# Performance work log

Measured on AMD Instinct MI355X. Metric: run time of the kernel, lower is better.

## Reference

```python
import jax, jax.numpy as jnp
import numpy as np

N_EMBED = 1024
CUTOFFS = [20000, 40000, 200000]
N_VOCAB = 267735
N_EMBEDS = [1024, 256, 64, 16]  # n_embed // 4**i
N_TOKENS = 1024
STARTS = [0] + CUTOFFS
ENDS = CUTOFFS + [N_VOCAB]


def setup_inputs() -> dict:
    key = jax.random.key(0)
    ks = jax.random.split(key, 16)
    s = 0.02
    inp = {}
    inp["hidden"] = jax.random.normal(ks[0], (N_TOKENS, N_EMBED), jnp.float32)
    inp["target"] = jax.random.randint(ks[1], (N_TOKENS,), 0, N_VOCAB)
    # head: layers[0] = Linear(1024, 20000); clusters = Linear(1024, 3)
    inp["W_head"] = jax.random.normal(ks[2], (ENDS[0], N_EMBEDS[0]), jnp.float32) * s
    inp["b_head"] = jax.random.normal(ks[3], (ENDS[0],), jnp.float32) * s
    inp["W_clusters"] = jax.random.normal(ks[4], (len(CUTOFFS), N_EMBED), jnp.float32) * s
    inp["b_clusters"] = jax.random.normal(ks[5], (len(CUTOFFS),), jnp.float32) * s
    # tails: projections[i-1] = Linear(1024, n_embeds[i], bias=False); layers[i] = Linear(n_embeds[i], end-start)
    k = 6
    for i in (1, 2, 3):
        d_i = N_EMBEDS[i]
        v_i = ENDS[i] - STARTS[i]
        inp[f"P{i}"] = jax.random.normal(ks[k], (d_i, N_EMBED), jnp.float32) * s
        inp[f"W{i}"] = jax.random.normal(ks[k + 1], (v_i, d_i), jnp.float32) * s
        inp[f"b{i}"] = jax.random.normal(ks[k + 2], (v_i,), jnp.float32) * s
        k += 3
    return inp


def reference(hidden, target, W_head, b_head, W_clusters, b_clusters,
              P1, W1, b1, P2, W2, b2, P3, W3, b3):
    # head logits: [N, cutoff0 + n_clusters]
    head_logit = jnp.concatenate(
        [hidden @ W_head.T + b_head, hidden @ W_clusters.T + b_clusters], axis=1)
    head_logprob = jax.nn.log_softmax(head_logit, axis=1)
    head_dim = head_logprob.shape[1]

    cuts = jnp.asarray(CUTOFFS)
    cluster_id = (target[:, None] >= cuts[None, :]).sum(axis=1)  # 0..3

    # cluster 0: direct head gather
    t0 = jnp.clip(target, 0, ENDS[0] - 1)
    lp0 = jnp.take_along_axis(head_logprob, t0[:, None], axis=1)[:, 0]

    def tail_lp(P, W, b, i):
        proj = hidden @ P.T                      # [N, d_i]
        tlp = jax.nn.log_softmax(proj @ W.T + b, axis=1)  # [N, v_i]
        ti = jnp.clip(target - STARTS[i], 0, W.shape[0] - 1)
        g = jnp.take_along_axis(tlp, ti[:, None], axis=1)[:, 0]
        # torch: head_logprob_i[:, -i]
        return head_logprob[:, head_dim - i] + g

    lp1 = tail_lp(P1, W1, b1, 1)
    lp2 = tail_lp(P2, W2, b2, 2)
    lp3 = tail_lp(P3, W3, b3, 3)

    logprob = jnp.select(
        [cluster_id == 0, cluster_id == 1, cluster_id == 2, cluster_id == 3],
        [lp0, lp1, lp2, lp3])
    return -logprob  # per-token NLL, keep_order ordering
```

## Files before the change

kernel.cpp:

```cpp
#include <hip/hip_runtime.h>
#include <cstdint>
#include <cstddef>

typedef __attribute__((ext_vector_type(8))) short short8;
typedef __attribute__((ext_vector_type(4))) float f32x4;

#define LOG2E 1.4426950408889634f
#define LN2   0.6931471805599453f

#define EXP2R(x) __builtin_amdgcn_exp2f(x)

__device__ __forceinline__ unsigned short f2bf(float x) {
    unsigned u = __float_as_uint(x);
    u += 0x7FFFu + ((u >> 16) & 1u);
    return (unsigned short)(u >> 16);
}
__device__ __forceinline__ float bf2f(unsigned short h) {
    return __uint_as_float(((unsigned)h) << 16);
}

__device__ __forceinline__ void gload_lds16(const void* g, void* l) {
    __builtin_amdgcn_global_load_lds(
        (const __attribute__((address_space(1))) unsigned int*)g,
        (__attribute__((address_space(3))) unsigned int*)l, 16, 0, 0);
}

__device__ __forceinline__ float sum16p(const f32x4 (&accv)[4][4], int ni,
                                        const float (&bvv)[4][4]) {
    float e[16];
#pragma unroll
    for (int q = 0; q < 16; ++q)
        e[q] = EXP2R(fmaf(accv[q >> 2][ni][q & 3], LOG2E, bvv[q >> 2][q & 3]));
#pragma unroll
    for (int st = 1; st < 16; st <<= 1)
#pragma unroll
        for (int q = 0; q < 16; q += st * 2)
            e[q] += e[q + st];
    return e[0];
}

__global__ void mega_convert(const float* __restrict__ hidden,
                             const float* __restrict__ P1, const float* __restrict__ P2,
                             const float* __restrict__ P3,
                             const float* __restrict__ W_head, const float* __restrict__ W_clu,
                             unsigned short* __restrict__ hbf, unsigned short* __restrict__ Pb,
                             unsigned short* __restrict__ Whb,
                             int nWh, int nClu, int nZp) {
    long i = (long)blockIdx.x * 256 + threadIdx.x;
    const float* src;
    unsigned short* dst;
    if (i < nWh)                      { src = W_head; dst = Whb; }
    else if ((i -= nWh) < nClu)       { src = W_clu;  dst = Whb + (size_t)20000 * 1024; }
    else if ((i -= nClu) < nZp) {
        *(unsigned long long*)(Whb + (size_t)20003 * 1024 + i * 4) = 0ull;
        return;
    }
    else if ((i -= nZp) < 262144)     { src = hidden; dst = hbf; }
    else if ((i -= 262144) < 65536)   { src = P1;     dst = Pb; }
    else if ((i -= 65536) < 16384)    { src = P2;     dst = Pb + (size_t)256 * 1024; }
    else if ((i -= 16384) < 4096)     { src = P3;     dst = Pb + (size_t)320 * 1024; }
    else if ((i -= 4096) < 12288) {
        *(unsigned long long*)(Pb + (size_t)336 * 1024 + i * 4) = 0ull;
        return;
    } else return;
    float4 v = *(const float4*)(src + (size_t)i * 4);
    unsigned long long p = (unsigned long long)f2bf(v.x)
                         | ((unsigned long long)f2bf(v.y) << 16)
                         | ((unsigned long long)f2bf(v.z) << 32)
                         | ((unsigned long long)f2bf(v.w) << 48);
    *(unsigned long long*)(dst + (size_t)i * 4) = p;
}

__global__ __launch_bounds__(1024)
void compact_tokens(const int* __restrict__ target, int* __restrict__ cnt,
                    int* __restrict__ slotc) {
    const int t = threadIdx.x;
    const int tgt = target[t];
    const int cid = (tgt >= 20000) + (tgt >= 40000) + (tgt >= 200000);
    const int wave = t >> 6, lane = t & 63;
    unsigned long long lt = (lane == 0) ? 0ull : (~0ull >> (64 - lane));
    __shared__ int wtot[3][16];
    __shared__ int wbase[3][16];
    unsigned long long bal[3];
#pragma unroll
    for (int c = 1; c <= 3; ++c) {
        unsigned long long b = __ballot(cid == c);
        if (lane == 0) wtot[c - 1][wave] = (int)__popcll(b);
        bal[c - 1] = b;
    }
    __syncthreads();
    if (t < 3) {
        int s = 0;
        for (int w = 0; w < 16; ++w) { wbase[t][w] = s; s += wtot[t][w]; }
        cnt[t + 1] = s;
        if (t == 0) cnt[0] = 1024;
    }
    __syncthreads();
    int sl = t;
    if (cid > 0) sl = wbase[cid - 1][wave] + (int)__popcll(bal[cid - 1] & lt);
    slotc[t] = sl | (cid << 16);
}

__global__ __launch_bounds__(256)
void proj_mfma(const unsigned short* __restrict__ Hb,
               const unsigned short* __restrict__ Pb,
               const int* __restrict__ slotc,
               unsigned short* __restrict__ Hc1,
               unsigned short* __restrict__ Hc2,
               unsigned short* __restrict__ Hc3) {
    __shared__ __align__(16) char As[16384];
    __shared__ __align__(16) char Bs[16384];
    __shared__ int sl_s[128];
    const int tid  = threadIdx.x;
    const int lane = tid & 63;
    const int wid  = tid >> 6;
    const int wm = wid >> 1, wn = wid & 1;
    const int tt = blockIdx.x, dt = blockIdx.y;
    const int t0 = tt * 128, d0 = dt * 128;

    f32x4 acc[4][4];
    const f32x4 zero = {0.f, 0.f, 0.f, 0.f};
#pragma unroll
    for (int i = 0; i < 4; ++i)
#pragma unroll
        for (int j = 0; j < 4; ++j) acc[i][j] = zero;

    const unsigned short* asrc[4];
    const unsigned short* bsrc[4];
    int ldst[4];
#pragma unroll
    for (int j = 0; j < 4; ++j) {
        int lds_off = wid * 4096 + j * 1024;
        int o = lds_off + lane * 16;
        int r = o >> 7;
        int b = (o & 127) ^ ((r & 7) << 4);
        ldst[j] = lds_off;
        asrc[j] = Hb + (size_t)(t0 + r) * 1024 + (b >> 1);
        bsrc[j] = Pb + (size_t)(d0 + r) * 1024 + (b >> 1);
    }

    for (int kt = 0; kt < 16; ++kt) {
#pragma unroll
        for (int j = 0; j < 4; ++j) gload_lds16(asrc[j] + kt * 64, As + ldst[j]);
#pragma unroll
        for (int j = 0; j < 4; ++j) gload_lds16(bsrc[j] + kt * 64, Bs + ldst[j]);
        __syncthreads();
#pragma unroll
        for (int kk = 0; kk < 2; ++kk) {
            const int kbyte = (kk * 32 + ((lane >> 4) << 3)) * 2;
            short8 a[4], b[4];
#pragma unroll
            for (int mi = 0; mi < 4; ++mi) {
                int row = wm * 64 + mi * 16 + (lane & 15);
                int off = row * 128 + (kbyte ^ ((row & 7) << 4));
                a[mi] = *(const short8*)(As + off);
            }
#pragma unroll
            for (int ni = 0; ni < 4; ++ni) {
                int row = wn * 64 + ni * 16 + (lane & 15);
                int off = row * 128 + (kbyte ^ ((row & 7) << 4));
                b[ni] = *(const short8*)(Bs + off);
            }
#pragma unroll
            for (int mi = 0; mi < 4; ++mi)
#pragma unroll
                for (int ni = 0; ni < 4; ++ni)
                    acc[mi][ni] = __builtin_amdgcn_mfma_f32_16x16x32_bf16(a[mi], b[ni], acc[mi][ni], 0, 0, 0);
        }
        __syncthreads();
    }

    if (tid < 128) sl_s[tid] = slotc[t0 + tid];
    __syncthreads();

#pragma unroll
    for (int ni = 0; ni < 4; ++ni) {
        int dg = d0 + wn * 64 + ni * 16 + (lane & 15);
        unsigned short* base;
        int c_d, dd, stride;
        if (dg < 256)      { c_d = 1; dd = dg;       base = Hc1; stride = 256; }
        else if (dg < 320) { c_d = 2; dd = dg - 256; base = Hc2; stride = 64;  }
        else               { c_d = 3; dd = dg - 320; base = Hc3; stride = 64;  }
#pragma unroll
        for (int mi = 0; mi < 4; ++mi)
#pragma unroll
            for (int r = 0; r < 4; ++r) {
                int tl = wm * 64 + mi * 16 + ((lane >> 4) << 2) + r;
                int sc = sl_s[tl];
                if ((sc >> 16) == c_d)
                    base[(size_t)(sc & 0xFFFF) * stride + dd] = f2bf(acc[mi][ni][r]);
            }
    }
}

template<bool BF16B>
__device__ __forceinline__ void gemm_lse_dev(
        char* Ws, char* Hs, float* bias_s, float* red,
        const unsigned short* __restrict__ Wb,
        const float* __restrict__ Wfa, const float* __restrict__ Wfb,
        int NsplitW, int NsplitB, int N, int K, int Kv, int KTILES,
        const float* __restrict__ bias1, const float* __restrict__ bias2,
        const unsigned short* __restrict__ H, int t0, int n0,
        float* __restrict__ pS_out) {
    const int tid  = threadIdx.x;
    const int lane = tid & 63;
    const int wid  = tid >> 6;
    const int wm = wid >> 1, wn = wid & 1;
    const bool clean = BF16B && (n0 + 128 <= NsplitW);

    if (tid < 128) {
        int v = n0 + tid;
        bias_s[tid] = (v < NsplitB) ? bias1[v] * LOG2E
                    : (v < N)       ? bias2[v - NsplitB] * LOG2E
                                    : -INFINITY;
    }

    f32x4 acc[4][4];
    const f32x4 zero = {0.f, 0.f, 0.f, 0.f};
#pragma unroll
    for (int i = 0; i < 4; ++i)
#pragma unroll
        for (int j = 0; j < 4; ++j) acc[i][j] = zero;

    const unsigned short* wsrc[4];
    const unsigned short* hsrc[4];
    int ldst[4];
#pragma unroll
    for (int j = 0; j < 4; ++j) {
        int lds_off = wid * 4096 + j * 1024;
        int o = lds_off + lane * 16;
        int r = o >> 7;
        int b = (o & 127) ^ ((r & 7) << 4);
        ldst[j] = lds_off;
        hsrc[j] = H + (size_t)(t0 + r) * K + (b >> 1);
        wsrc[j] = clean ? (Wb + (size_t)(n0 + r) * K + (b >> 1)) : nullptr;
    }
    int arow[4], brow[4];
#pragma unroll
    for (int q = 0; q < 4; ++q) {
        arow[q] = wm * 64 + q * 16 + (lane & 15);
        brow[q] = wn * 64 + q * 16 + (lane & 15);
    }
    const int kbase = (lane >> 4) << 4;

    for (int kt = 0; kt < KTILES; ++kt) {
        if (clean) {
#pragma unroll
            for (int j = 0; j < 4; ++j) gload_lds16(wsrc[j] + kt * 64, Ws + ldst[j]);
        } else {
#pragma unroll
            for (int it = 0; it < 4; ++it) {
                int c = tid + it * 256;
                int row = c >> 3, kc = (c & 7) << 3;
                int v = n0 + row;
                int kg = kt * 64 + kc;
                unsigned short hh[8] = {0,0,0,0,0,0,0,0};
                if (v < NsplitB) {
                    if (BF16B) {
                        *(int4*)hh = *(const int4*)(Wb + (size_t)v * K + kg);
                    } else if (kg + 8 <= Kv) {
                        const float* p = Wfa + (size_t)v * Kv;
                        float4 u0 = *(const float4*)(p + kg);
                        float4 u1 = *(const float4*)(p + kg + 4);
                        hh[0]=f2bf(u0.x); hh[1]=f2bf(u0.y); hh[2]=f2bf(u0.z); hh[3]=f2bf(u0.w);
                        hh[4]=f2bf(u1.x); hh[5]=f2bf(u1.y); hh[6]=f2bf(u1.z); hh[7]=f2bf(u1.w);
                    }
                } else if (v < N && Wfb != nullptr) {
                    const float* p = Wfb + (size_t)(v - NsplitB) * K;
                    float4 u0 = *(const float4*)(p + kg);
                    float4 u1 = *(const float4*)(p + kg + 4);
                    hh[0]=f2bf(u0.x); hh[1]=f2bf(u0.y); hh[2]=f2bf(u0.z); hh[3]=f2bf(u0.w);
                    hh[4]=f2bf(u1.x); hh[5]=f2bf(u1.y); hh[6]=f2bf(u1.z); hh[7]=f2bf(u1.w);
                }
                int off = (row * 128 + kc * 2) ^ ((row & 7) << 4);
                *(int4*)(Ws + off) = *(const int4*)hh;
            }
        }
#pragma unroll
        for (int j = 0; j < 4; ++j) gload_lds16(hsrc[j] + kt * 64, Hs + ldst[j]);
        __syncthreads();
#pragma unroll
        for (int kk = 0; kk < 2; ++kk) {
            const int kbyte = kk * 64 + kbase;
            short8 a[4], b[4];
#pragma unroll
            for (int mi = 0; mi < 4; ++mi)
                a[mi] = *(const short8*)(Ws + arow[mi] * 128 + (kbyte ^ ((arow[mi] & 7) << 4)));
#pragma unroll
            for (int ni = 0; ni < 4; ++ni)
                b[ni] = *(const short8*)(Hs + brow[ni] * 128 + (kbyte ^ ((brow[ni] & 7) << 4)));
#pragma unroll
            for (int mi = 0; mi < 4; ++mi)
#pragma unroll
                for (int ni = 0; ni < 4; ++ni)
                    acc[mi][ni] = __builtin_amdgcn_mfma_f32_16x16x32_bf16(a[mi], b[ni], acc[mi][ni], 0, 0, 0);
        }
        __syncthreads();
    }

    float bvv[4][4];
#pragma unroll
    for (int mi = 0; mi < 4; ++mi)
#pragma unroll
        for (int r = 0; r < 4; ++r)
            bvv[mi][r] = bias_s[wm * 64 + mi * 16 + ((lane >> 4) << 2) + r];

    const int gslot = (wm * 4 + (lane >> 4)) * 128 + wn * 64 + (lane & 15);
#pragma unroll
    for (int ni = 0; ni < 4; ++ni)
        red[gslot + ni * 16] = sum16p(acc, ni, bvv);
    __syncthreads();
    if (tid < 128) {
        float s = 0.f;
#pragma unroll
        for (int g = 0; g < 8; ++g) s += red[g * 128 + tid];
        pS_out[t0 + tid] = s;
    }
}

template<int KV>
__device__ __forceinline__ void tail_res_dev(
        char* Ws, char* Hs, float* bias_s, float* red,
        const float* __restrict__ Wf, int N,
        const float* __restrict__ bias,
        const unsigned short* __restrict__ Hc, int cntc, int n0,
        float* __restrict__ pS_out) {
    const int tid = threadIdx.x, lane = tid & 63, wid = tid >> 6;
    const int wm = wid >> 1, wn = wid & 1;

#pragma unroll
    for (int it = 0; it < 4; ++it) {
        int c = tid + it * 256;
        int row = c >> 3, kc = (c & 7) << 3;
        int v = n0 + row;
        unsigned short hh[8] = {0,0,0,0,0,0,0,0};
        if (v < N && kc < KV) {
            const float* p = Wf + (size_t)v * KV + kc;
            float4 u0 = *(const float4*)p;
            float4 u1 = *(const float4*)(p + 4);
            hh[0]=f2bf(u0.x); hh[1]=f2bf(u0.y); hh[2]=f2bf(u0.z); hh[3]=f2bf(u0.w);
            hh[4]=f2bf(u1.x); hh[5]=f2bf(u1.y); hh[6]=f2bf(u1.z); hh[7]=f2bf(u1.w);
        }
        int off = (row * 128 + kc * 2) ^ ((row & 7) << 4);
        *(int4*)(Ws + off) = *(const int4*)hh;
    }
    if (tid < 128) {
        int v = n0 + tid;
        bias_s[tid] = (v < N) ? bias[v] * LOG2E : -INFINITY;
    }
    __syncthreads();
    short8 a[2][4];
#pragma unroll
    for (int kk = 0; kk < 2; ++kk)
#pragma unroll
        for (int mi = 0; mi < 4; ++mi) {
            int row = wm * 64 + mi * 16 + (lane & 15);
            int kbyte = (kk * 32 + ((lane >> 4) << 3)) * 2;
            a[kk][mi] = *(const short8*)(Ws + ((row * 128 + kbyte) ^ ((row & 7) << 4)));
        }
    float bvv[4][4];
#pragma unroll
    for (int mi = 0; mi < 4; ++mi)
#pragma unroll
        for (int r = 0; r < 4; ++r)
            bvv[mi][r] = bias_s[wm * 64 + mi * 16 + ((lane >> 4) << 2) + r];
    const int ntt = (cntc + 127) >> 7;

    const unsigned short* hsrc[4];
    int ldst[4];
#pragma unroll
    for (int j = 0; j < 4; ++j) {
        int lds_off = wid * 4096 + j * 1024;
        int o = lds_off + lane * 16;
        int r = o >> 7;
        int b = (o & 127) ^ ((r & 7) << 4);
        ldst[j] = lds_off;
        hsrc[j] = Hc + (size_t)r * 64 + (b >> 1);
    }
    int brow[4];
#pragma unroll
    for (int q = 0; q < 4; ++q) brow[q] = wn * 64 + q * 16 + (lane & 15);
    const int kbase = (lane >> 4) << 4;
    const int gslot = (wm * 4 + (lane >> 4)) * 128 + wn * 64 + (lane & 15);

    for (int tt = 0; tt < ntt; ++tt) {
#pragma unroll
        for (int j = 0; j < 4; ++j)
            gload_lds16(hsrc[j] + tt * 8192, Hs + ldst[j]);
        __syncthreads();
        f32x4 acc[4][4];
        const f32x4 zero = {0.f, 0.f, 0.f, 0.f};
#pragma unroll
        for (int i = 0; i < 4; ++i)
#pragma unroll
            for (int j = 0; j < 4; ++j) acc[i][j] = zero;
#pragma unroll
        for (int kk = 0; kk < 2; ++kk) {
            const int kbyte = kk * 64 + kbase;
            short8 b[4];
#pragma unroll
            for (int ni = 0; ni < 4; ++ni)
                b[ni] = *(const short8*)(Hs + brow[ni] * 128 + (kbyte ^ ((brow[ni] & 7) << 4)));
#pragma unroll
            for (int mi = 0; mi < 4; ++mi)
#pragma unroll
                for (int ni = 0; ni < 4; ++ni)
                    acc[mi][ni] = __builtin_amdgcn_mfma_f32_16x16x32_bf16(a[kk][mi], b[ni], acc[mi][ni], 0, 0, 0);
        }
#pragma unroll
        for (int ni = 0; ni < 4; ++ni)
            red[gslot + ni * 16] = sum16p(acc, ni, bvv);
        __syncthreads();
        if (tid < 128) {
            float s = 0.f;
#pragma unroll
            for (int g = 0; g < 8; ++g) s += red[g * 128 + tid];
            pS_out[tt * 128 + tid] = s;
        }
    }
}

#define NSLOT 435
template<bool PRE>
__global__ __launch_bounds__(256)
void fused_lse(const unsigned short* __restrict__ Whb,
               const float* __restrict__ W_head, const float* __restrict__ W_clu,
               const float* __restrict__ W1,
               const float* __restrict__ W2, const float* __restrict__ W3,
               const float* __restrict__ b_head, const float* __restrict__ b_clu,
               const float* __restrict__ b1, const float* __restrict__ b2,
               const float* __restrict__ b3,
               const unsigned short* __restrict__ hbf,
               const unsigned short* __restrict__ Hc1,
               const unsigned short* __restrict__ Hc2,
               const unsigned short* __restrict__ Hc3,
               const int* __restrict__ cnt,
               float* __restrict__ pSh, float* __restrict__ pS1,
               float* __restrict__ pS2, float* __restrict__ pS3) {
    __shared__ __align__(16) char smem[37376];
    char* Ws = smem;
    char* Hs = smem + 16384;
    float* bias_s = (float*)(smem + 32768);
    float* red    = (float*)(smem + 33280);
    const int b = blockIdx.x;
    const int x = b & 7;
    const int i = b >> 3;
    const int m = i % 5, j = i / 5;

    if (m == 0 || m == 2) {
        const int h = 2 * j + (m >> 1);
        if (h >= 160) return;
        const int nt = x * 20 + (h >> 3);
        const int tt = h & 7;
        if (nt >= 157) return;
        if (PRE)
            gemm_lse_dev<true>(Ws, Hs, bias_s, red,
                               Whb, nullptr, nullptr,
                               20096, 20000, 20003, 1024, 1024, 16,
                               b_head, b_clu, hbf, tt * 128, nt * 128,
                               pSh + (size_t)nt * 1024);
        else
            gemm_lse_dev<false>(Ws, Hs, bias_s, red,
                                nullptr, W_head, W_clu,
                                20000, 20000, 20003, 1024, 1024, 16,
                                b_head, b_clu, hbf, tt * 128, nt * 128,
                                pSh + (size_t)nt * 1024);
    } else if (m == 1 || m == 3) {
        const int v = (2 * j + ((m - 1) >> 1)) * 8 + x;
        if (v >= 1250) return;
        tail_res_dev<64>(Ws, Hs, bias_s, red, W2, 160000, b2,
                         Hc2, cnt[2], v * 128, pS2 + (size_t)v * 1024);
    } else {
        if (j < 67) {
            const int v = j * 8 + x;
            if (v >= 530) return;
            tail_res_dev<16>(Ws, Hs, bias_s, red, W3, 67735, b3,
                             Hc3, cnt[3], v * 128, pS3 + (size_t)v * 1024);
        } else {
            const int nt = (j - 67) * 8 + x;
            if (nt >= 157) return;
            const int c1 = cnt[1];
            for (int t0 = 0; t0 < c1; t0 += 128)
                gemm_lse_dev<false>(Ws, Hs, bias_s, red,
                                    nullptr, W1, nullptr,
                                    20000, 20000, 20000, 256, 256, 4,
                                    b1, nullptr, Hc1, t0, nt * 128,
                                    pS1 + (size_t)nt * 1024);
        }
    }
}

__global__ __launch_bounds__(256)
void reduce_part(const float* __restrict__ pSh, int nth,
                 const float* __restrict__ pS1, int nt1,
                 const float* __restrict__ pS2, int nt2,
                 const float* __restrict__ pS3, int nt3,
                 float* __restrict__ pRs) {
    const int c = blockIdx.y, z = blockIdx.z;
    const float* PS = (c == 0) ? pSh : (c == 1) ? pS1 : (c == 2) ? pS2 : pS3;
    const int nt = (c == 0) ? nth : (c == 1) ? nt1 : (c == 2) ? nt2 : nt3;
    const int lane = threadIdx.x & 63;
    const int seg  = threadIdx.x >> 6;
    const int t = blockIdx.x * 64 + lane;
    float s = 0.f;
    for (int i = z * 4 + seg; i < nt; i += 64)
        s += PS[(size_t)i * 1024 + t];
    __shared__ float rs[4][64];
    rs[seg][lane] = s;
    __syncthreads();
    if (seg == 0) {
        s += rs[1][lane] + rs[2][lane] + rs[3][lane];
        pRs[((size_t)c * 16 + z) * 1024 + t] = s;
    }
}

__global__ void finalize(const float* __restrict__ hidden, const int* __restrict__ target,
                         const float* __restrict__ W_head, const float* __restrict__ b_head,
                         const float* __restrict__ W_clu, const float* __restrict__ b_clu,
                         const float* __restrict__ W1, const float* __restrict__ b1,
                         const float* __restrict__ W2, const float* __restrict__ b2,
                         const float* __restrict__ W3, const float* __restrict__ b3,
                         const unsigned short* __restrict__ Hc1,
                         const unsigned short* __restrict__ Hc2,
                         const unsigned short* __restrict__ Hc3,
                         const int* __restrict__ slotc,
                         const float* __restrict__ pRs,
                         float* __restrict__ out) {
    const int t = blockIdx.x;
    const int lane = threadIdx.x;
    const int tgt = target[t];
    const int cid = (tgt >= 20000) + (tgt >= 40000) + (tgt >= 200000);
    const int slot = slotc[t] & 0xFFFF;

    float v = 0.f;
    if (lane < 16)
        v = pRs[(size_t)lane * 1024 + t];
    else if (lane < 32 && cid > 0)
        v = pRs[((size_t)cid * 16 + (lane - 16)) * 1024 + slot];
#pragma unroll
    for (int msk = 1; msk < 16; msk <<= 1) v += __shfl_xor(v, msk, 64);
    float lse0 = LN2 * log2f(__shfl(v, 0, 64));
    float lsec = (cid > 0) ? LN2 * log2f(__shfl(v, 16, 64)) : 0.f;

    const int j = (cid == 0) ? tgt : (20003 - cid);
    const float* wr = (j < 20000) ? (W_head + (size_t)j * 1024)
                                  : (W_clu + (size_t)(j - 20000) * 1024);
    float acc = 0.f;
#pragma unroll
    for (int i = 0; i < 4; ++i) {
        int k4 = lane + i * 64;
        float4 h = *(const float4*)(hidden + (size_t)t * 1024 + k4 * 4);
        float4 w = *(const float4*)(wr + k4 * 4);
        acc += h.x * w.x + h.y * w.y + h.z * w.z + h.w * w.w;
    }
#pragma unroll
    for (int msk = 1; msk < 64; msk <<= 1) acc += __shfl_xor(acc, msk, 64);
    float bj = (j < 20000) ? b_head[j] : b_clu[j - 20000];
    float res = (acc + bj) - lse0;
    if (cid > 0) {
        const int starts[4] = {0, 20000, 40000, 200000};
        const int dims[4]   = {0, 256, 64, 16};
        const float* Wt = (cid == 1) ? W1 : (cid == 2) ? W2 : W3;
        const float* bt = (cid == 1) ? b1 : (cid == 2) ? b2 : b3;
        const unsigned short* pr = (cid == 1) ? Hc1 + (size_t)slot * 256
                                 : (cid == 2) ? Hc2 + (size_t)slot * 64
                                              : Hc3 + (size_t)slot * 64;
        int ti = tgt - starts[cid];
        int d  = dims[cid];
        const float* wt = Wt + (size_t)ti * d;
        float a2 = 0.f;
        for (int k = lane; k < d; k += 64) a2 += bf2f(pr[k]) * wt[k];
#pragma unroll
        for (int msk = 1; msk < 64; msk <<= 1) a2 += __shfl_xor(a2, msk, 64);
        res += (a2 + bt[ti]) - lsec;
    }
    if (lane == 0) out[t] = -res;
}

extern "C" void kernel_launch(void* const* d_in, const int* in_sizes, int n_in,
                              void* d_out, int out_size, void* d_ws, size_t ws_size,
                              hipStream_t stream) {
    const float* hidden = (const float*)d_in[0];
    const int*   target = (const int*)d_in[1];
    const float* W_head = (const float*)d_in[2];
    const float* b_head = (const float*)d_in[3];
    const float* W_clu  = (const float*)d_in[4];
    const float* b_clu  = (const float*)d_in[5];
    const float* P1 = (const float*)d_in[6];
    const float* W1 = (const float*)d_in[7];
    const float* b1 = (const float*)d_in[8];
    const float* P2 = (const float*)d_in[9];
    const float* W2 = (const float*)d_in[10];
    const float* b2 = (const float*)d_in[11];
    const float* P3 = (const float*)d_in[12];
    const float* W3 = (const float*)d_in[13];
    const float* b3 = (const float*)d_in[14];
    float* out = (float*)d_out;

    char* ws = (char*)d_ws;
    size_t off = 0;
    auto alloc = [&](size_t bytes) -> char* {
        char* p = ws + off;
        off += (bytes + 255) & ~(size_t)255;
        return p;
    };
    const int NT_H = 157;
    const int NT_1 = 157;
    const int NT_2 = 1250;
    const int NT_3 = 530;

    unsigned short* hbf   = (unsigned short*)alloc((size_t)1024 * 1024 * 2);
    unsigned short* Pb    = (unsigned short*)alloc((size_t)384 * 1024 * 2);
    int* cnt   = (int*)alloc(4 * 4);
    int* slotc = (int*)alloc(1024 * 4);
    unsigned short* Hc1 = (unsigned short*)alloc((size_t)1024 * 256 * 2);
    unsigned short* Hc2 = (unsigned short*)alloc((size_t)1024 * 64 * 2);
    unsigned short* Hc3 = (unsigned short*)alloc((size_t)1024 * 64 * 2);
    float* pSh = (float*)alloc((size_t)1024 * NT_H * 4);
    float* pS1 = (float*)alloc((size_t)1024 * NT_1 * 4);
    float* pS2 = (float*)alloc((size_t)1024 * NT_2 * 4);
    float* pS3 = (float*)alloc((size_t)1024 * NT_3 * 4);
    float* pRs = (float*)alloc((size_t)4 * 16 * 1024 * 4);
    unsigned short* Whb = (unsigned short*)alloc((size_t)20096 * 1024 * 2);
    const bool pre = (off <= ws_size);

    const int nWh  = pre ? 5120000 : 0;
    const int nClu = pre ? 768 : 0;
    const int nZp  = pre ? 23808 : 0;
    const long nChunks = (long)nWh + nClu + nZp + 360448;
    mega_convert<<<(unsigned)((nChunks + 255) / 256), 256, 0, stream>>>(
        hidden, P1, P2, P3, W_head, W_clu, hbf, Pb, Whb, nWh, nClu, nZp);
    compact_tokens<<<1, 1024, 0, stream>>>(target, cnt, slotc);
    proj_mfma<<<dim3(8, 3), 256, 0, stream>>>(hbf, Pb, slotc, Hc1, Hc2, Hc3);

    const int NB_TOT = 8 * NSLOT;
    if (pre)
        fused_lse<true><<<NB_TOT, 256, 0, stream>>>(
            Whb, W_head, W_clu, W1, W2, W3,
            b_head, b_clu, b1, b2, b3,
            hbf, Hc1, Hc2, Hc3, cnt, pSh, pS1, pS2, pS3);
    else
        fused_lse<false><<<NB_TOT, 256, 0, stream>>>(
            Whb, W_head, W_clu, W1, W2, W3,
            b_head, b_clu, b1, b2, b3,
            hbf, Hc1, Hc2, Hc3, cnt, pSh, pS1, pS2, pS3);

    reduce_part<<<dim3(16, 4, 16), 256, 0, stream>>>(pSh, NT_H, pS1, NT_1,
                                                     pS2, NT_2, pS3, NT_3, pRs);

    finalize<<<1024, 64, 0, stream>>>(hidden, target,
                                      W_head, b_head, W_clu, b_clu,
                                      W1, b1, W2, b2, W3, b3,
                                      Hc1, Hc2, Hc3, slotc, pRs, out);
}
```

Baseline: 150.2 us.

## Replace partial-sum buffers and reduce kernel with atomic accumulation

```diff
diff --git a/kernel.cpp b/kernel.cpp
--- a/kernel.cpp
+++ b/kernel.cpp
@@ -7,6 +7,7 @@
 
 #define LOG2E 1.4426950408889634f
 #define LN2   0.6931471805599453f
+#define RSTR  144
 
 #define EXP2R(x) __builtin_amdgcn_exp2f(x)
 
@@ -201,7 +202,7 @@
         int NsplitW, int NsplitB, int N, int K, int Kv, int KTILES,
         const float* __restrict__ bias1, const float* __restrict__ bias2,
         const unsigned short* __restrict__ H, int t0, int n0,
-        float* __restrict__ pS_out) {
+        float* __restrict__ pT) {
     const int tid  = threadIdx.x;
     const int lane = tid & 63;
     const int wid  = tid >> 6;
@@ -305,7 +306,7 @@
         for (int r = 0; r < 4; ++r)
             bvv[mi][r] = bias_s[wm * 64 + mi * 16 + ((lane >> 4) << 2) + r];
 
-    const int gslot = (wm * 4 + (lane >> 4)) * 128 + wn * 64 + (lane & 15);
+    const int gslot = (wm * 4 + (lane >> 4)) * RSTR + wn * 64 + (lane & 15);
 #pragma unroll
     for (int ni = 0; ni < 4; ++ni)
         red[gslot + ni * 16] = sum16p(acc, ni, bvv);
@@ -313,8 +314,8 @@
     if (tid < 128) {
         float s = 0.f;
 #pragma unroll
-        for (int g = 0; g < 8; ++g) s += red[g * 128 + tid];
-        pS_out[t0 + tid] = s;
+        for (int g = 0; g < 8; ++g) s += red[g * RSTR + tid];
+        atomicAdd(&pT[t0 + tid], s);
     }
 }
 
@@ -324,7 +325,7 @@
         const float* __restrict__ Wf, int N,
         const float* __restrict__ bias,
         const unsigned short* __restrict__ Hc, int cntc, int n0,
-        float* __restrict__ pS_out) {
+        float* __restrict__ pT) {
     const int tid = threadIdx.x, lane = tid & 63, wid = tid >> 6;
     const int wm = wid >> 1, wn = wid & 1;
 
@@ -381,7 +382,7 @@
 #pragma unroll
     for (int q = 0; q < 4; ++q) brow[q] = wn * 64 + q * 16 + (lane & 15);
     const int kbase = (lane >> 4) << 4;
-    const int gslot = (wm * 4 + (lane >> 4)) * 128 + wn * 64 + (lane & 15);
+    const int gslot = (wm * 4 + (lane >> 4)) * RSTR + wn * 64 + (lane & 15);
 
     for (int tt = 0; tt < ntt; ++tt) {
 #pragma unroll
@@ -414,8 +415,8 @@
         if (tid < 128) {
             float s = 0.f;
 #pragma unroll
-            for (int g = 0; g < 8; ++g) s += red[g * 128 + tid];
-            pS_out[tt * 128 + tid] = s;
+            for (int g = 0; g < 8; ++g) s += red[g * RSTR + tid];
+            atomicAdd(&pT[tt * 128 + tid], s);
         }
     }
 }
@@ -435,9 +436,8 @@
                const unsigned short* __restrict__ Hc2,
                const unsigned short* __restrict__ Hc3,
                const int* __restrict__ cnt,
-               float* __restrict__ pSh, float* __restrict__ pS1,
-               float* __restrict__ pS2, float* __restrict__ pS3) {
-    __shared__ __align__(16) char smem[37376];
+               float* __restrict__ pT) {
+    __shared__ __align__(16) char smem[37888];
     char* Ws = smem;
     char* Hs = smem + 16384;
     float* bias_s = (float*)(smem + 32768);
@@ -457,25 +457,23 @@
             gemm_lse_dev<true>(Ws, Hs, bias_s, red,
                                Whb, nullptr, nullptr,
                                20096, 20000, 20003, 1024, 1024, 16,
-                               b_head, b_clu, hbf, tt * 128, nt * 128,
-                               pSh + (size_t)nt * 1024);
+                               b_head, b_clu, hbf, tt * 128, nt * 128, pT);
         else
             gemm_lse_dev<false>(Ws, Hs, bias_s, red,
                                 nullptr, W_head, W_clu,
                                 20000, 20000, 20003, 1024, 1024, 16,
-                                b_head, b_clu, hbf, tt * 128, nt * 128,
-                                pSh + (size_t)nt * 1024);
+                                b_head, b_clu, hbf, tt * 128, nt * 128, pT);
     } else if (m == 1 || m == 3) {
         const int v = (2 * j + ((m - 1) >> 1)) * 8 + x;
         if (v >= 1250) return;
         tail_res_dev<64>(Ws, Hs, bias_s, red, W2, 160000, b2,
-                         Hc2, cnt[2], v * 128, pS2 + (size_t)v * 1024);
+                         Hc2, cnt[2], v * 128, pT + 2 * 1024);
     } else {
         if (j < 67) {
             const int v = j * 8 + x;
             if (v >= 530) return;
             tail_res_dev<16>(Ws, Hs, bias_s, red, W3, 67735, b3,
-                             Hc3, cnt[3], v * 128, pS3 + (size_t)v * 1024);
+                             Hc3, cnt[3], v * 128, pT + 3 * 1024);
         } else {
             const int nt = (j - 67) * 8 + x;
             if (nt >= 157) return;
@@ -484,33 +482,8 @@
                 gemm_lse_dev<false>(Ws, Hs, bias_s, red,
                                     nullptr, W1, nullptr,
                                     20000, 20000, 20000, 256, 256, 4,
-                                    b1, nullptr, Hc1, t0, nt * 128,
-                                    pS1 + (size_t)nt * 1024);
-        }
-    }
-}
-
-__global__ __launch_bounds__(256)
-void reduce_part(const float* __restrict__ pSh, int nth,
-                 const float* __restrict__ pS1, int nt1,
-                 const float* __restrict__ pS2, int nt2,
-                 const float* __restrict__ pS3, int nt3,
-                 float* __restrict__ pRs) {
-    const int c = blockIdx.y, z = blockIdx.z;
-    const float* PS = (c == 0) ? pSh : (c == 1) ? pS1 : (c == 2) ? pS2 : pS3;
-    const int nt = (c == 0) ? nth : (c == 1) ? nt1 : (c == 2) ? nt2 : nt3;
-    const int lane = threadIdx.x & 63;
-    const int seg  = threadIdx.x >> 6;
-    const int t = blockIdx.x * 64 + lane;
-    float s = 0.f;
-    for (int i = z * 4 + seg; i < nt; i += 64)
-        s += PS[(size_t)i * 1024 + t];
-    __shared__ float rs[4][64];
-    rs[seg][lane] = s;
-    __syncthreads();
-    if (seg == 0) {
-        s += rs[1][lane] + rs[2][lane] + rs[3][lane];
-        pRs[((size_t)c * 16 + z) * 1024 + t] = s;
+                                    b1, nullptr, Hc1, t0, nt * 128, pT + 1 * 1024);
+        }
     }
 }
 
@@ -524,7 +497,7 @@
                          const unsigned short* __restrict__ Hc2,
                          const unsigned short* __restrict__ Hc3,
                          const int* __restrict__ slotc,
-                         const float* __restrict__ pRs,
+                         const float* __restrict__ pT,
                          float* __restrict__ out) {
     const int t = blockIdx.x;
     const int lane = threadIdx.x;
@@ -532,15 +505,8 @@
     const int cid = (tgt >= 20000) + (tgt >= 40000) + (tgt >= 200000);
     const int slot = slotc[t] & 0xFFFF;
 
-    float v = 0.f;
-    if (lane < 16)
-        v = pRs[(size_t)lane * 1024 + t];
-    else if (lane < 32 && cid > 0)
-        v = pRs[((size_t)cid * 16 + (lane - 16)) * 1024 + slot];
-#pragma unroll
-    for (int msk = 1; msk < 16; msk <<= 1) v += __shfl_xor(v, msk, 64);
-    float lse0 = LN2 * log2f(__shfl(v, 0, 64));
-    float lsec = (cid > 0) ? LN2 * log2f(__shfl(v, 16, 64)) : 0.f;
+    float lse0 = LN2 * log2f(pT[t]);
+    float lsec = (cid > 0) ? LN2 * log2f(pT[cid * 1024 + slot]) : 0.f;
 
     const int j = (cid == 0) ? tgt : (20003 - cid);
     const float* wr = (j < 20000) ? (W_head + (size_t)j * 1024)
@@ -604,10 +570,6 @@
         off += (bytes + 255) & ~(size_t)255;
         return p;
     };
-    const int NT_H = 157;
-    const int NT_1 = 157;
-    const int NT_2 = 1250;
-    const int NT_3 = 530;
 
     unsigned short* hbf   = (unsigned short*)alloc((size_t)1024 * 1024 * 2);
     unsigned short* Pb    = (unsigned short*)alloc((size_t)384 * 1024 * 2);
@@ -616,11 +578,7 @@
     unsigned short* Hc1 = (unsigned short*)alloc((size_t)1024 * 256 * 2);
     unsigned short* Hc2 = (unsigned short*)alloc((size_t)1024 * 64 * 2);
     unsigned short* Hc3 = (unsigned short*)alloc((size_t)1024 * 64 * 2);
-    float* pSh = (float*)alloc((size_t)1024 * NT_H * 4);
-    float* pS1 = (float*)alloc((size_t)1024 * NT_1 * 4);
-    float* pS2 = (float*)alloc((size_t)1024 * NT_2 * 4);
-    float* pS3 = (float*)alloc((size_t)1024 * NT_3 * 4);
-    float* pRs = (float*)alloc((size_t)4 * 16 * 1024 * 4);
+    float* pT  = (float*)alloc((size_t)4 * 1024 * 4);
     unsigned short* Whb = (unsigned short*)alloc((size_t)20096 * 1024 * 2);
     const bool pre = (off <= ws_size);
 
@@ -631,6 +589,7 @@
     mega_convert<<<(unsigned)((nChunks + 255) / 256), 256, 0, stream>>>(
         hidden, P1, P2, P3, W_head, W_clu, hbf, Pb, Whb, nWh, nClu, nZp);
     compact_tokens<<<1, 1024, 0, stream>>>(target, cnt, slotc);
+    (void)hipMemsetAsync(pT, 0, (size_t)4 * 1024 * 4, stream);
     proj_mfma<<<dim3(8, 3), 256, 0, stream>>>(hbf, Pb, slotc, Hc1, Hc2, Hc3);
 
     const int NB_TOT = 8 * NSLOT;
@@ -638,18 +597,15 @@
         fused_lse<true><<<NB_TOT, 256, 0, stream>>>(
             Whb, W_head, W_clu, W1, W2, W3,
             b_head, b_clu, b1, b2, b3,
-            hbf, Hc1, Hc2, Hc3, cnt, pSh, pS1, pS2, pS3);
+            hbf, Hc1, Hc2, Hc3, cnt, pT);
     else
         fused_lse<false><<<NB_TOT, 256, 0, stream>>>(
             Whb, W_head, W_clu, W1, W2, W3,
             b_head, b_clu, b1, b2, b3,
-            hbf, Hc1, Hc2, Hc3, cnt, pSh, pS1, pS2, pS3);
-
-    reduce_part<<<dim3(16, 4, 16), 256, 0, stream>>>(pSh, NT_H, pS1, NT_1,
-                                                     pS2, NT_2, pS3, NT_3, pRs);
+            hbf, Hc1, Hc2, Hc3, cnt, pT);
 
     finalize<<<1024, 64, 0, stream>>>(hidden, target,
                                       W_head, b_head, W_clu, b_clu,
                                       W1, b1, W2, b2, W3, b3,
-                                      Hc1, Hc2, Hc3, slotc, pRs, out);
-}
+                                      Hc1, Hc2, Hc3, slotc, pT, out);
+}
```

Measured after the change: 149.0 us, median of 2. About the same (-0.8%).
